# Optimization experiments

Hardware: AMD Instinct MI355X
Metric: run time of the kernel (lower is better)

The kernel has to match this reference:

```python
import jax, jax.numpy as jnp
import numpy as np
import math

B, L, M, N, S = 1024, 32, 128, 4096, 32


def setup_inputs() -> dict:
    key = jax.random.key(0)
    k1, k2, k3 = jax.random.split(key, 3)
    k = jax.random.normal(k1, (B, L, M), dtype=jnp.float32)
    # kaiming-uniform-like init: U(-bound, bound)
    bound_e = math.sqrt(6.0 / (N * M))
    bound_d = math.sqrt(6.0 / (M * N))
    W_e = jax.random.uniform(k2, (L, N, M), dtype=jnp.float32, minval=-bound_e, maxval=bound_e)
    W_d = jax.random.uniform(k3, (L, M, N), dtype=jnp.float32, minval=-bound_d, maxval=bound_d)
    # decoder columns are unit-normalized along the m axis (dim=-2), as in __init__
    W_d = W_d / jnp.linalg.norm(W_d, axis=-2, keepdims=True)
    b_e = jnp.zeros((L, N), dtype=jnp.float32)
    b_d = jnp.zeros((L, M), dtype=jnp.float32)
    return {"k": k, "W_e": W_e, "b_e": b_e, "W_d": W_d, "b_d": b_d, "s": S}


def hard_thresholding(y, s):
    # keep the s largest-|.| activations per (batch, layer) row, zero the rest
    _, idx = jax.lax.top_k(jnp.abs(y), s)  # idx: [B, L, s]
    b, l, _ = y.shape
    mask = jnp.zeros_like(y).at[
        jnp.arange(b)[:, None, None], jnp.arange(l)[None, :, None], idx
    ].set(1.0)
    return y * mask


def reference(k, W_e, b_e, W_d, b_d, s):
    # NOTE: b_e is created by the module but (faithfully) unused in encode()
    k_bar = k - b_d                                  # [B, L, M]
    y = jnp.einsum('lnm,blm->bln', W_e, k_bar)        # [B, L, N]
    y = hard_thresholding(y, s)
    k_hat = jnp.einsum('lmn,bln->blm', W_d, y)        # [B, L, M]
    loss = jnp.mean((k_hat - k) ** 2)
    return (loss, k_hat, y)
```

## Files before the change

kernel.cpp:

```cpp
#include <hip/hip_runtime.h>
#include <hip/hip_bf16.h>

#define B_ 1024
#define L_ 32
#define M_ 128
#define N_ 4096
#define S_ 32
#define ROWS (B_ * L_)

typedef __attribute__((ext_vector_type(8))) short    short8_t;
typedef __attribute__((ext_vector_type(8))) unsigned short ushort8_t;
typedef __attribute__((ext_vector_type(4))) float    f32x4;

__device__ __forceinline__ unsigned short f2bf(float x) {
    unsigned u = __float_as_uint(x);
    unsigned r = (u + 0x7FFFu + ((u >> 16) & 1u)) >> 16;
    return (unsigned short)r;
}
__device__ __forceinline__ float bf2f(unsigned short h) {
    return __uint_as_float((unsigned)h << 16);
}

__global__ __launch_bounds__(256) void transpose_wd(const float* __restrict__ Wd,
                                                    float* __restrict__ WdT) {
    __shared__ float t[32][33];
    int l = blockIdx.z;
    int n0 = blockIdx.x * 32, m0 = blockIdx.y * 32;
    int tx = threadIdx.x & 31, ty = threadIdx.x >> 5;
    const float* src = Wd + (size_t)l * M_ * N_;
    for (int i = ty; i < 32; i += 8)
        t[i][tx] = src[(size_t)(m0 + i) * N_ + n0 + tx];
    __syncthreads();
    float* dst = WdT + (size_t)l * N_ * M_;
    for (int i = ty; i < 32; i += 8)
        dst[(size_t)(n0 + i) * M_ + m0 + tx] = t[tx][i];
}

__global__ __launch_bounds__(256) void zero_y_low(float* __restrict__ y) {
    const float4 z = {0.f, 0.f, 0.f, 0.f};
    int idx = blockIdx.x * 256 + threadIdx.x;
    for (int i = idx; i < ROWS * 512; i += 2048 * 256) {
        int row = i >> 9, slot = i & 511;
        reinterpret_cast<float4*>(y + (size_t)row * N_)[slot] = z;
    }
}

__global__ __launch_bounds__(256) void zero_y_high(float* __restrict__ y) {
    const float4 z = {0.f, 0.f, 0.f, 0.f};
    int idx = blockIdx.x * 256 + threadIdx.x;
    for (int i = idx; i < ROWS * 512; i += 2048 * 256) {
        int row = i >> 9, slot = i & 511;
        reinterpret_cast<float4*>(y + (size_t)row * N_ + 2048)[slot] = z;
    }
}

__global__ __launch_bounds__(256) void scatter_high(float* __restrict__ y,
                                                    const int* __restrict__ cidx,
                                                    const float* __restrict__ cval) {
    int g = blockIdx.x * 256 + threadIdx.x;
    int row = g >> 5;
    int n = cidx[g];
    if (n >= 2048) y[(size_t)row * N_ + n] = cval[g];
}

__global__ __launch_bounds__(256) void prep_w(const float* __restrict__ We,
                                              const float* __restrict__ bd,
                                              unsigned short* __restrict__ Wbf,
                                              float* __restrict__ cvec) {
    int l = blockIdx.y;
    int tid = threadIdx.x;
    int nl = tid >> 4, t = tid & 15;
    int n = blockIdx.x * 16 + nl;
    const float* w = We + ((size_t)l * N_ + n) * M_ + t * 8;
    const float* b = bd + l * M_ + t * 8;
    float4 w0 = *(const float4*)(w), w1 = *(const float4*)(w + 4);
    float4 b0 = *(const float4*)(b), b1 = *(const float4*)(b + 4);
    ushort8_t o;
    o[0] = f2bf(w0.x); o[1] = f2bf(w0.y); o[2] = f2bf(w0.z); o[3] = f2bf(w0.w);
    o[4] = f2bf(w1.x); o[5] = f2bf(w1.y); o[6] = f2bf(w1.z); o[7] = f2bf(w1.w);
    *reinterpret_cast<ushort8_t*>(Wbf + ((size_t)l * N_ + n) * 128 + t * 8) = o;
    float s = w0.x*b0.x + w0.y*b0.y + w0.z*b0.z + w0.w*b0.w
            + w1.x*b1.x + w1.y*b1.y + w1.z*b1.z + w1.w*b1.w;
    #pragma unroll
    for (int oo = 8; oo > 0; oo >>= 1) s += __shfl_xor(s, oo, 64);
    if (t == 0) cvec[(size_t)l * N_ + n] = s;
}

__global__ __launch_bounds__(256) void prep_a(const float* __restrict__ kin,
                                              unsigned short* __restrict__ Abf) {
    int g = blockIdx.x * 256 + threadIdx.x;
    int b = g >> 12, l = (g >> 7) & 31, m = g & 127;
    Abf[(((size_t)l * B_ + b) << 7) + m] = f2bf(kin[g]);
}

__device__ __forceinline__ int swz(int row) { return (row & 3) ^ ((row >> 2) & 3); }

#define CP 136

__global__ __launch_bounds__(256) void encoder_mfma(const unsigned short* __restrict__ Abf,
                                                    const unsigned short* __restrict__ Wbf,
                                                    const float* __restrict__ cvec,
                                                    unsigned short* __restrict__ y16) {
    const int l   = blockIdx.z;
    const int bn0 = blockIdx.x * 128;
    const int bm0 = blockIdx.y * 128;
    __shared__ __align__(16) unsigned short smem[128 * CP];
    unsigned short* As = smem;
    unsigned short* Bs = smem + 128 * 32;
    const int tid  = threadIdx.x;
    const int lane = tid & 63, wave = tid >> 6;
    const int wr = wave >> 1, wc = wave & 1;

    const unsigned short* Ab = Abf + (((size_t)l * B_ + bm0) << 7);
    const unsigned short* Wb = Wbf + (((size_t)l * N_ + bn0) << 7);

    auto stage = [&](int k0) {
        #pragma unroll
        for (int i = 0; i < 2; ++i) {
            int p   = i * 256 + tid;
            int row = p >> 2;
            int lc  = (p & 3) ^ swz(row);
            const unsigned short* g = Ab + ((size_t)row << 7) + k0 + lc * 8;
            unsigned dst = (unsigned)((i * 256 + (tid & ~63)) * 16);
            __builtin_amdgcn_global_load_lds(
                (const __attribute__((address_space(1))) void*)g,
                (__attribute__((address_space(3))) void*)((char*)As + dst), 16, 0, 0);
        }
        #pragma unroll
        for (int i = 0; i < 2; ++i) {
            int p   = i * 256 + tid;
            int row = p >> 2;
            int lc  = (p & 3) ^ swz(row);
            const unsigned short* g = Wb + ((size_t)row << 7) + k0 + lc * 8;
            unsigned dst = (unsigned)((i * 256 + (tid & ~63)) * 16);
            __builtin_amdgcn_global_load_lds(
                (const __attribute__((address_space(1))) void*)g,
                (__attribute__((address_space(3))) void*)((char*)Bs + dst), 16, 0, 0);
        }
    };

    f32x4 acc[4][4];
    #pragma unroll
    for (int i = 0; i < 4; ++i)
        #pragma unroll
        for (int j = 0; j < 4; ++j) acc[i][j] = (f32x4){0.f, 0.f, 0.f, 0.f};

    stage(0);
    __syncthreads();

    #pragma unroll
    for (int t = 0; t < 4; ++t) {
        short8_t aF[4], bF[4];
        const int kg = lane >> 4;
        #pragma unroll
        for (int mt = 0; mt < 4; ++mt) {
            int row = wr * 64 + mt * 16 + (lane & 15);
            int pc  = kg ^ swz(row);
            aF[mt] = *reinterpret_cast<const short8_t*>(As + row * 32 + pc * 8);
        }
        #pragma unroll
        for (int nt = 0; nt < 4; ++nt) {
            int row = wc * 64 + nt * 16 + (lane & 15);
            int pc  = kg ^ swz(row);
            bF[nt] = *reinterpret_cast<const short8_t*>(Bs + row * 32 + pc * 8);
        }
        #pragma unroll
        for (int mt = 0; mt < 4; ++mt)
            #pragma unroll
            for (int nt = 0; nt < 4; ++nt)
                acc[mt][nt] = __builtin_amdgcn_mfma_f32_16x16x32_bf16(
                    aF[mt], bF[nt], acc[mt][nt], 0, 0, 0);

        if (t < 3) {
            __syncthreads();
            stage((t + 1) * 32);
            __syncthreads();
        }
    }

    __syncthreads();

    #pragma unroll
    for (int nt = 0; nt < 4; ++nt) {
        int nl = wc * 64 + nt * 16 + (lane & 15);
        float cj = cvec[(size_t)l * N_ + bn0 + nl];
        #pragma unroll
        for (int mt = 0; mt < 4; ++mt) {
            #pragma unroll
            for (int j = 0; j < 4; ++j) {
                int rl = wr * 64 + mt * 16 + (lane >> 4) * 4 + j;
                smem[rl * CP + nl] = f2bf(acc[mt][nt][j] - cj);
            }
        }
    }
    __syncthreads();

    #pragma unroll
    for (int i = 0; i < 8; ++i) {
        int chunk = i * 256 + tid;
        int r = chunk >> 4, cch = chunk & 15;
        ushort8_t v = *reinterpret_cast<const ushort8_t*>(smem + r * CP + cch * 8);
        unsigned short* dst = y16 + ((size_t)((bm0 + r) * L_ + l)) * 8192 + 4096 + bn0 + cch * 8;
        *reinterpret_cast<ushort8_t*>(dst) = v;
    }
}

#define POOL 96
#define MARGIN 1.2e-3f

__global__ __launch_bounds__(256) void topk_decode(float* __restrict__ y,
                                                   const float* __restrict__ We,
                                                   const float* __restrict__ WdT,
                                                   const float* __restrict__ kin,
                                                   const float* __restrict__ cvec,
                                                   int* __restrict__ cidx,
                                                   float* __restrict__ cval,
                                                   float* __restrict__ khat,
                                                   float* __restrict__ partial) {
    const int w    = threadIdx.x >> 6;
    const int lane = threadIdx.x & 63;
    const int wid  = (blockIdx.x << 2) + w;
    const int l = wid >> 10, b = wid & 1023;
    const int row = b * L_ + l;

    __shared__ __align__(16) float kinS[4][M_];
    __shared__ int   pidxS[4][POOL];
    __shared__ float pexS[4][POOL];
    __shared__ int   sidxS[4][S_];
    __shared__ float svalS[4][S_];

    float* yo = y + (size_t)row * N_;
    const unsigned short* ya = (const unsigned short*)y + (size_t)row * 8192 + 4096;

    kinS[w][lane]      = kin[(size_t)row * M_ + lane];
    kinS[w][lane + 64] = kin[(size_t)row * M_ + lane + 64];

    ushort8_t u[8];
    #pragma unroll
    for (int j = 0; j < 8; ++j)
        u[j] = *reinterpret_cast<const ushort8_t*>(ya + j * 512 + lane * 8);
    float a[64];
    #pragma unroll
    for (int j = 0; j < 8; ++j)
        #pragma unroll
        for (int e = 0; e < 8; ++e)
            a[j * 8 + e] = fabsf(bf2f(u[j][e]));

    float mx = 0.0f, s1 = 0.0f, s2 = 0.0f;
    #pragma unroll
    for (int i = 0; i < 64; ++i) {
        mx = fmaxf(mx, a[i]);
        s1 += a[i];
        s2 = fmaf(a[i], a[i], s2);
    }
    #pragma unroll
    for (int o = 32; o > 0; o >>= 1) {
        mx = fmaxf(mx, __shfl_xor(mx, o, 64));
        s1 += __shfl_xor(s1, o, 64);
        s2 += __shfl_xor(s2, o, 64);
    }
    const float mu  = s1 * (1.0f / 4096.0f);
    const float var = fmaxf(s2 * (1.0f / 4096.0f) - mu * mu, 0.0f);
    const float sg  = sqrtf(var);

    float lo = 0.0f, hi = mx;
    int cl = N_;
    for (int it = 0; it < 30 && cl > 40; ++it) {
        float t;
        if      (it == 0) t = mu + 2.20f * sg;
        else if (it == 1) t = mu + 2.96f * sg;
        else              t = 0.5f * (lo + hi);
        t = fminf(fmaxf(t, lo), hi);
        int c = 0;
        #pragma unroll
        for (int i = 0; i < 64; ++i) c += (a[i] >= t) ? 1 : 0;
        #pragma unroll
        for (int o = 32; o > 0; o >>= 1) c += __shfl_xor(c, o, 64);
        if (c >= S_) { lo = t; cl = c; } else { hi = t; }
    }

    const float th = lo - MARGIN;
    int myc = 0;
    #pragma unroll
    for (int i = 0; i < 64; ++i) myc += (a[i] >= th) ? 1 : 0;
    int pos = myc;
    #pragma unroll
    for (int o = 1; o < 64; o <<= 1) {
        int t = __shfl_up(pos, o, 64);
        if (lane >= o) pos += t;
    }
    const int base  = pos - myc;
    const int total = __shfl(pos, 63, 64);
    int k = 0;
    #pragma unroll
    for (int j = 0; j < 8; ++j)
        #pragma unroll
        for (int e = 0; e < 8; ++e)
            if (a[j * 8 + e] >= th) {
                int p = base + k;
                if (p < POOL) pidxS[w][p] = j * 512 + lane * 8 + e;
                ++k;
            }
    __asm__ __volatile__("s_waitcnt lgkmcnt(0)" ::: "memory");
    int c = total < POOL ? total : POOL;

    if (lane < c) {
        int n = pidxS[w][lane];
        const float4* wp4 = reinterpret_cast<const float4*>(We + ((size_t)l * N_ + n) * M_);
        const float4* kp4 = reinterpret_cast<const float4*>(kinS[w]);
        float acc = -cvec[(size_t)l * N_ + n];
        #pragma unroll 8
        for (int m4 = 0; m4 < 32; ++m4) {
            float4 wv = wp4[m4], kv = kp4[m4];
            acc = fmaf(wv.x, kv.x, acc);
            acc = fmaf(wv.y, kv.y, acc);
            acc = fmaf(wv.z, kv.z, acc);
            acc = fmaf(wv.w, kv.w, acc);
        }
        pexS[w][lane] = acc;
    }
    if (lane + 64 < c) {
        int n = pidxS[w][lane + 64];
        const float4* wp4 = reinterpret_cast<const float4*>(We + ((size_t)l * N_ + n) * M_);
        const float4* kp4 = reinterpret_cast<const float4*>(kinS[w]);
        float acc = -cvec[(size_t)l * N_ + n];
        #pragma unroll 8
        for (int m4 = 0; m4 < 32; ++m4) {
            float4 wv = wp4[m4], kv = kp4[m4];
            acc = fmaf(wv.x, kv.x, acc);
            acc = fmaf(wv.y, kv.y, acc);
            acc = fmaf(wv.z, kv.z, acc);
            acc = fmaf(wv.w, kv.w, acc);
        }
        pexS[w][lane + 64] = acc;
    }
    __asm__ __volatile__("s_waitcnt lgkmcnt(0)" ::: "memory");

    for (int e = lane; e < c; e += 64) {
        float ae = fabsf(pexS[w][e]);
        int   ne = pidxS[w][e];
        int rank = 0;
        for (int j = 0; j < c; ++j) {
            float aj = fabsf(pexS[w][j]);
            rank += ((aj > ae) || (aj == ae && pidxS[w][j] < ne)) ? 1 : 0;
        }
        if (rank < S_) {
            sidxS[w][rank] = ne;
            svalS[w][rank] = pexS[w][e];
        }
    }
    __asm__ __volatile__("s_waitcnt lgkmcnt(0)" ::: "memory");

    if (lane < S_) {
        int n = sidxS[w][lane];
        float v = svalS[w][lane];
        cidx[(size_t)row * S_ + lane] = n;
        cval[(size_t)row * S_ + lane] = v;
        if (n < 2048) yo[n] = v;
    }

    const float* wt = WdT + (size_t)l * N_ * M_;
    float acc0 = 0.0f, acc1 = 0.0f;
    #pragma unroll 4
    for (int j = 0; j < S_; ++j) {
        float v = svalS[w][j];
        const float* wrp = wt + (size_t)sidxS[w][j] * M_;
        acc0 = fmaf(v, wrp[lane], acc0);
        acc1 = fmaf(v, wrp[lane + 64], acc1);
    }
    khat[(size_t)row * M_ + lane]      = acc0;
    khat[(size_t)row * M_ + lane + 64] = acc1;
    float r0 = acc0 - kinS[w][lane];
    float r1 = acc1 - kinS[w][lane + 64];
    float s = r0 * r0 + r1 * r1;
    #pragma unroll
    for (int o = 32; o > 0; o >>= 1) s += __shfl_xor(s, o, 64);
    if (lane == 0) partial[row] = s;
}

__global__ __launch_bounds__(256) void reduce_loss(const float* __restrict__ partial,
                                                   float* __restrict__ out_loss) {
    __shared__ float red[256];
    int tid = threadIdx.x;
    float s = 0.0f;
    for (int i = tid; i < ROWS / 4; i += 256) {
        float4 v = reinterpret_cast<const float4*>(partial)[i];
        s += v.x + v.y + v.z + v.w;
    }
    red[tid] = s;
    __syncthreads();
    for (int off = 128; off > 0; off >>= 1) {
        if (tid < off) red[tid] += red[tid + off];
        __syncthreads();
    }
    if (tid == 0) out_loss[0] = red[0] / (float)((size_t)B_ * L_ * M_);
}

extern "C" void kernel_launch(void* const* d_in, const int* in_sizes, int n_in,
                              void* d_out, int out_size, void* d_ws, size_t ws_size,
                              hipStream_t stream) {
    const float* kin = (const float*)d_in[0];
    const float* We  = (const float*)d_in[1];
    const float* Wd  = (const float*)d_in[3];
    const float* bd  = (const float*)d_in[4];

    float* out   = (float*)d_out;
    float* loss  = out;
    float* khat  = out + 1;
    float* y_out = out + 1 + (size_t)B_ * L_ * M_;

    char* ws = (char*)d_ws;
    unsigned short* Wbf = (unsigned short*)ws;
    float*          WdT = (float*)ws;
    unsigned short* Abf = (unsigned short*)(ws + (64u << 20));
    int*   cidx    = (int*)  (ws + (72u << 20));
    float* cval    = (float*)(ws + (76u << 20));
    float* cvec    = (float*)(ws + (80u << 20));
    float* partial = (float*)(ws + (81u << 20));

    zero_y_low<<<2048, 256, 0, stream>>>(y_out);
    prep_w<<<dim3(N_ / 16, L_), 256, 0, stream>>>(We, bd, Wbf, cvec);
    prep_a<<<(B_ * L_ * M_) / 256, 256, 0, stream>>>(kin, Abf);
    encoder_mfma<<<dim3(N_ / 128, B_ / 128, L_), 256, 0, stream>>>(
        Abf, Wbf, cvec, (unsigned short*)y_out);
    transpose_wd<<<dim3(N_ / 32, M_ / 32, L_), 256, 0, stream>>>(Wd, WdT);
    topk_decode<<<ROWS / 4, 256, 0, stream>>>(y_out, We, WdT, kin, cvec,
                                              cidx, cval, khat, partial);
    zero_y_high<<<2048, 256, 0, stream>>>(y_out);
    scatter_high<<<(ROWS * S_) / 256, 256, 0, stream>>>(y_out, cidx, cval);
    reduce_loss<<<1, 256, 0, stream>>>(partial, loss);
}
```

Before: 584.3 us.

## Merge prologue kernels and fuse high-half zeroing with scatter

Four prologue kernels (zero low half of y, weight bf16 prep, activation bf16 prep, and the decoder-weight transpose) become one launch with block-index dispatch. When the workspace is large enough, WdT goes to a separate region so the transpose can run before the encoder instead of after it. Zeroing the high half of y and scattering the top-k values into it are fused into one per-row-group kernel. The decode loop unroll factor also goes from 4 to 8. The aim is fewer launches and less serialization, at the cost of a branchy mixed-work kernel and an extra workspace requirement.

After: 588.2 us. Within noise of the previous version (+0.7%).

```diff
diff --git a/kernel.cpp b/kernel.cpp
--- a/kernel.cpp
+++ b/kernel.cpp
@@ -19,6 +19,64 @@
 }
 __device__ __forceinline__ float bf2f(unsigned short h) {
     return __uint_as_float((unsigned)h << 16);
+}
+
+__global__ __launch_bounds__(256) void prologue(float* __restrict__ y,
+                                                const float* __restrict__ We,
+                                                const float* __restrict__ bd,
+                                                unsigned short* __restrict__ Wbf,
+                                                float* __restrict__ cvec,
+                                                const float* __restrict__ kin,
+                                                unsigned short* __restrict__ Abf,
+                                                const float* __restrict__ Wd,
+                                                float* __restrict__ WdT) {
+    __shared__ float t[32][33];
+    const int bid = blockIdx.x;
+    const int tid = threadIdx.x;
+
+    if (bid < 2048) {
+        const float4 z = {0.f, 0.f, 0.f, 0.f};
+        int idx = bid * 256 + tid;
+        for (int i = idx; i < ROWS * 512; i += 2048 * 256) {
+            int row = i >> 9, slot = i & 511;
+            reinterpret_cast<float4*>(y + (size_t)row * N_)[slot] = z;
+        }
+    } else if (bid < 10240) {
+        int wb = bid - 2048;
+        int l = wb >> 8, nb = wb & 255;
+        int nl = tid >> 4, tt = tid & 15;
+        int n = nb * 16 + nl;
+        const float* w = We + ((size_t)l * N_ + n) * M_ + tt * 8;
+        const float* b = bd + l * M_ + tt * 8;
+        float4 w0 = *(const float4*)(w), w1 = *(const float4*)(w + 4);
+        float4 b0 = *(const float4*)(b), b1 = *(const float4*)(b + 4);
+        ushort8_t o;
+        o[0] = f2bf(w0.x); o[1] = f2bf(w0.y); o[2] = f2bf(w0.z); o[3] = f2bf(w0.w);
+        o[4] = f2bf(w1.x); o[5] = f2bf(w1.y); o[6] = f2bf(w1.z); o[7] = f2bf(w1.w);
+        *reinterpret_cast<ushort8_t*>(Wbf + ((size_t)l * N_ + n) * 128 + tt * 8) = o;
+        float s = w0.x*b0.x + w0.y*b0.y + w0.z*b0.z + w0.w*b0.w
+                + w1.x*b1.x + w1.y*b1.y + w1.z*b1.z + w1.w*b1.w;
+        #pragma unroll
+        for (int oo = 8; oo > 0; oo >>= 1) s += __shfl_xor(s, oo, 64);
+        if (tt == 0) cvec[(size_t)l * N_ + n] = s;
+    } else if (bid < 26624) {
+        int g = (bid - 10240) * 256 + tid;
+        int b = g >> 12, l = (g >> 7) & 31, m = g & 127;
+        Abf[(((size_t)l * B_ + b) << 7) + m] = f2bf(kin[g]);
+    } else {
+        int tb = bid - 26624;
+        int l  = tb >> 9;
+        int rem = tb & 511;
+        int n0 = (rem & 127) * 32, m0 = (rem >> 7) * 32;
+        int tx = tid & 31, ty = tid >> 5;
+        const float* src = Wd + (size_t)l * M_ * N_;
+        for (int i = ty; i < 32; i += 8)
+            t[i][tx] = src[(size_t)(m0 + i) * N_ + n0 + tx];
+        __syncthreads();
+        float* dst = WdT + (size_t)l * N_ * M_;
+        for (int i = ty; i < 32; i += 8)
+            dst[(size_t)(n0 + i) * M_ + m0 + tx] = t[tx][i];
+    }
 }
 
 __global__ __launch_bounds__(256) void transpose_wd(const float* __restrict__ Wd,
@@ -34,63 +92,6 @@
     float* dst = WdT + (size_t)l * N_ * M_;
     for (int i = ty; i < 32; i += 8)
         dst[(size_t)(n0 + i) * M_ + m0 + tx] = t[tx][i];
-}
-
-__global__ __launch_bounds__(256) void zero_y_low(float* __restrict__ y) {
-    const float4 z = {0.f, 0.f, 0.f, 0.f};
-    int idx = blockIdx.x * 256 + threadIdx.x;
-    for (int i = idx; i < ROWS * 512; i += 2048 * 256) {
-        int row = i >> 9, slot = i & 511;
-        reinterpret_cast<float4*>(y + (size_t)row * N_)[slot] = z;
-    }
-}
-
-__global__ __launch_bounds__(256) void zero_y_high(float* __restrict__ y) {
-    const float4 z = {0.f, 0.f, 0.f, 0.f};
-    int idx = blockIdx.x * 256 + threadIdx.x;
-    for (int i = idx; i < ROWS * 512; i += 2048 * 256) {
-        int row = i >> 9, slot = i & 511;
-        reinterpret_cast<float4*>(y + (size_t)row * N_ + 2048)[slot] = z;
-    }
-}
-
-__global__ __launch_bounds__(256) void scatter_high(float* __restrict__ y,
-                                                    const int* __restrict__ cidx,
-                                                    const float* __restrict__ cval) {
-    int g = blockIdx.x * 256 + threadIdx.x;
-    int row = g >> 5;
-    int n = cidx[g];
-    if (n >= 2048) y[(size_t)row * N_ + n] = cval[g];
-}
-
-__global__ __launch_bounds__(256) void prep_w(const float* __restrict__ We,
-                                              const float* __restrict__ bd,
-                                              unsigned short* __restrict__ Wbf,
-                                              float* __restrict__ cvec) {
-    int l = blockIdx.y;
-    int tid = threadIdx.x;
-    int nl = tid >> 4, t = tid & 15;
-    int n = blockIdx.x * 16 + nl;
-    const float* w = We + ((size_t)l * N_ + n) * M_ + t * 8;
-    const float* b = bd + l * M_ + t * 8;
-    float4 w0 = *(const float4*)(w), w1 = *(const float4*)(w + 4);
-    float4 b0 = *(const float4*)(b), b1 = *(const float4*)(b + 4);
-    ushort8_t o;
-    o[0] = f2bf(w0.x); o[1] = f2bf(w0.y); o[2] = f2bf(w0.z); o[3] = f2bf(w0.w);
-    o[4] = f2bf(w1.x); o[5] = f2bf(w1.y); o[6] = f2bf(w1.z); o[7] = f2bf(w1.w);
-    *reinterpret_cast<ushort8_t*>(Wbf + ((size_t)l * N_ + n) * 128 + t * 8) = o;
-    float s = w0.x*b0.x + w0.y*b0.y + w0.z*b0.z + w0.w*b0.w
-            + w1.x*b1.x + w1.y*b1.y + w1.z*b1.z + w1.w*b1.w;
-    #pragma unroll
-    for (int oo = 8; oo > 0; oo >>= 1) s += __shfl_xor(s, oo, 64);
-    if (t == 0) cvec[(size_t)l * N_ + n] = s;
-}
-
-__global__ __launch_bounds__(256) void prep_a(const float* __restrict__ kin,
-                                              unsigned short* __restrict__ Abf) {
-    int g = blockIdx.x * 256 + threadIdx.x;
-    int b = g >> 12, l = (g >> 7) & 31, m = g & 127;
-    Abf[(((size_t)l * B_ + b) << 7) + m] = f2bf(kin[g]);
 }
 
 __device__ __forceinline__ int swz(int row) { return (row & 3) ^ ((row >> 2) & 3); }
@@ -361,7 +362,7 @@
 
     const float* wt = WdT + (size_t)l * N_ * M_;
     float acc0 = 0.0f, acc1 = 0.0f;
-    #pragma unroll 4
+    #pragma unroll 8
     for (int j = 0; j < S_; ++j) {
         float v = svalS[w][j];
         const float* wrp = wt + (size_t)sidxS[w][j] * M_;
@@ -376,6 +377,33 @@
     #pragma unroll
     for (int o = 32; o > 0; o >>= 1) s += __shfl_xor(s, o, 64);
     if (lane == 0) partial[row] = s;
+}
+
+__global__ __launch_bounds__(256) void finish_high(float* __restrict__ y,
+                                                   const int* __restrict__ cidx,
+                                                   const float* __restrict__ cval) {
+    const int bid = blockIdx.x;
+    const int tid = threadIdx.x;
+    const int row0 = bid * 16;
+    const float4 z = {0.f, 0.f, 0.f, 0.f};
+    #pragma unroll
+    for (int i = 0; i < 32; ++i) {
+        int g = i * 256 + tid;
+        int r = row0 + (g >> 9);
+        int slot = g & 511;
+        reinterpret_cast<float4*>(y + (size_t)r * N_ + 2048)[slot] = z;
+    }
+    __syncthreads();
+    #pragma unroll
+    for (int i = 0; i < 2; ++i) {
+        int e = i * 256 + tid;
+        int g = row0 * S_ + e;
+        int n = cidx[g];
+        if (n >= 2048) {
+            int r = row0 + (e >> 5);
+            y[(size_t)r * N_ + n] = cval[g];
+        }
+    }
 }
 
 __global__ __launch_bounds__(256) void reduce_loss(const float* __restrict__ partial,
@@ -411,22 +439,23 @@
 
     char* ws = (char*)d_ws;
     unsigned short* Wbf = (unsigned short*)ws;
-    float*          WdT = (float*)ws;
     unsigned short* Abf = (unsigned short*)(ws + (64u << 20));
     int*   cidx    = (int*)  (ws + (72u << 20));
     float* cval    = (float*)(ws + (76u << 20));
     float* cvec    = (float*)(ws + (80u << 20));
     float* partial = (float*)(ws + (81u << 20));
-
-    zero_y_low<<<2048, 256, 0, stream>>>(y_out);
-    prep_w<<<dim3(N_ / 16, L_), 256, 0, stream>>>(We, bd, Wbf, cvec);
-    prep_a<<<(B_ * L_ * M_) / 256, 256, 0, stream>>>(kin, Abf);
+    const bool wsBig = ws_size >= ((size_t)146u << 20);
+    float* WdT = wsBig ? (float*)(ws + ((size_t)82u << 20))
+                       : (float*)ws;
+
+    int nblocks = 26624 + (wsBig ? 16384 : 0);
+    prologue<<<nblocks, 256, 0, stream>>>(y_out, We, bd, Wbf, cvec, kin, Abf, Wd, WdT);
     encoder_mfma<<<dim3(N_ / 128, B_ / 128, L_), 256, 0, stream>>>(
         Abf, Wbf, cvec, (unsigned short*)y_out);
-    transpose_wd<<<dim3(N_ / 32, M_ / 32, L_), 256, 0, stream>>>(Wd, WdT);
+    if (!wsBig)
+        transpose_wd<<<dim3(N_ / 32, M_ / 32, L_), 256, 0, stream>>>(Wd, WdT);
     topk_decode<<<ROWS / 4, 256, 0, stream>>>(y_out, We, WdT, kin, cvec,
                                               cidx, cval, khat, partial);
-    zero_y_high<<<2048, 256, 0, stream>>>(y_out);
-    scatter_high<<<(ROWS * S_) / 256, 256, 0, stream>>>(y_out, cidx, cval);
+    finish_high<<<2048, 256, 0, stream>>>(y_out, cidx, cval);
     reduce_loss<<<1, 256, 0, stream>>>(partial, loss);
 }
```
